# Kernel optimization log

Measured on AMD Instinct MI355X. Metric: run time of the kernel, lower is better.

The kernel has to match this reference:

```python
import jax, jax.numpy as jnp
import numpy as np

N_NODES = 50000
N_EDGES = 800000
IN_FEATS = 256
HEADS = 4
OUT_FEATS = 32
NEG_SLOPE = 0.2


def setup_inputs() -> dict:
    key = jax.random.key(0)
    ks = jax.random.split(key, 8)
    return {
        "feat": jax.random.normal(ks[0], (N_NODES, IN_FEATS), dtype=jnp.float32),
        "edge_weight": jax.random.uniform(ks[1], (N_EDGES,), dtype=jnp.float32),
        "src": jax.random.randint(ks[2], (N_EDGES,), 0, N_NODES, dtype=jnp.int32),
        "dst": jax.random.randint(ks[3], (N_EDGES,), 0, N_NODES, dtype=jnp.int32),
        "W_fc": jax.random.normal(ks[4], (HEADS * OUT_FEATS, IN_FEATS), dtype=jnp.float32) * 0.05,
        "W_edge": jax.random.normal(ks[5], (HEADS * OUT_FEATS, 1), dtype=jnp.float32) * 0.05,
        "attn_l": jax.random.normal(ks[6], (1, HEADS, OUT_FEATS), dtype=jnp.float32) * 0.1,
        "attn_r": jax.random.normal(ks[7], (1, HEADS, OUT_FEATS), dtype=jnp.float32) * 0.1,
        "bias": jnp.zeros((HEADS * OUT_FEATS,), dtype=jnp.float32),
    }


def reference(feat, edge_weight, src, dst, W_fc, W_edge, attn_l, attn_r, bias):
    N = feat.shape[0]
    H, F = attn_l.shape[1], attn_l.shape[2]
    # node projection: [N, H, F]
    feat_hf = (feat @ W_fc.T).reshape(N, H, F)
    el = jnp.sum(feat_hf * attn_l, axis=-1)  # [N, H]
    er = jnp.sum(feat_hf * attn_r, axis=-1)  # [N, H]
    # edgefc(weight.unsqueeze(-1)): Linear(1, H*F) -> weight[e] * W_edge[:,0]
    edge_ft = (edge_weight[:, None] * W_edge[:, 0][None, :]).reshape(-1, H, F)  # [E,H,F]
    # e = leaky_relu(u_add_v(el, er) + edge_ft); broadcast [E,H,1] + [E,H,F]
    e = (el[src] + er[dst])[:, :, None] + edge_ft
    e = jnp.where(e >= 0, e, NEG_SLOPE * e)
    # edge softmax per destination (elementwise over H, F)
    m = jax.ops.segment_max(e, dst, num_segments=N)  # [N,H,F]
    m = jnp.where(jnp.isfinite(m), m, 0.0)
    ex = jnp.exp(e - m[dst])
    s = jax.ops.segment_sum(ex, dst, num_segments=N)  # [N,H,F]
    a = ex / s[dst]
    # weighted aggregation: sum_{e: dst=v} ft[src[e]] * a[e]
    rst = jax.ops.segment_sum(feat_hf[src] * a, dst, num_segments=N)  # [N,H,F]
    rst = rst + bias.reshape(1, H, F)
    return rst
```

## Files before the change

kernel.cpp:

```cpp
#include <hip/hip_runtime.h>

#define NN 50000
#define NE 800000
#define KF 256
#define HF 128
#define NEG 0.2f
#define INVLN2 1.44269504088896340736f

#define NB 391
#define EB 391
#define EPB 2048
#define PREP_BLOCKS 64
#define PROJ_BLOCKS 782
#define ELR_BLOCKS 12500

typedef __attribute__((ext_vector_type(8))) short bf16x8;
typedef __attribute__((ext_vector_type(4))) float f32x4;

static __device__ __forceinline__ unsigned bf16_rne(float x) {
  unsigned u = __float_as_uint(x);
  return (u + 0x7fffu + ((u >> 16) & 1u)) >> 16;
}
static __device__ __forceinline__ unsigned cvt_pk(float lo, float hi) {
  unsigned r;
  asm("v_cvt_pk_bf16_f32 %0, %1, %2" : "=v"(r) : "v"(lo), "v"(hi));
  return r;
}
static __device__ __forceinline__ float exp2_raw(float x) {
  float r;
  asm("v_exp_f32 %0, %1" : "=v"(r) : "v"(x));
  return r;
}

__global__ __launch_bounds__(256) void k1_prep_hist(
    const float* __restrict__ Wfc, unsigned* __restrict__ wfcb,
    const int* __restrict__ dst, unsigned short* __restrict__ rank16,
    int* __restrict__ histE) {
  if (blockIdx.x < PREP_BLOCKS) {
    int t = blockIdx.x * 256 + threadIdx.x;
    int e2 = t & 3;
    int l  = (t >> 2) & 63;
    int ct = (t >> 8) & 7;
    int ks = t >> 11;
    int j = ct * 16 + (l & 15);
    int k = ks * 32 + (l >> 4) * 8 + 2 * e2;
    unsigned lo = bf16_rne(Wfc[j * KF + k]);
    unsigned hi = bf16_rne(Wfc[j * KF + k + 1]);
    wfcb[t] = lo | (hi << 16);
    return;
  }
  int e = blockIdx.x - PREP_BLOCKS;
  __shared__ int hist[NB];
  for (int b = threadIdx.x; b < NB; b += 256) hist[b] = 0;
  __syncthreads();
  int base = e * EPB;
  int cnt = min(EPB, NE - base);
  for (int k = threadIdx.x; k < cnt; k += 256) {
    int d = dst[base + k];
    int r = atomicAdd(&hist[d >> 7], 1);
    rank16[base + k] = (unsigned short)r;
  }
  __syncthreads();
  for (int b = threadIdx.x; b < NB; b += 256) histE[e * NB + b] = hist[b];
}

__global__ __launch_bounds__(256) void k2_proj_scan(
    const float* __restrict__ feat, const unsigned* __restrict__ wfcb,
    unsigned* __restrict__ ftp, const int* __restrict__ histE,
    int* __restrict__ colbase, int* __restrict__ bucketTotal) {
  if (blockIdx.x >= PROJ_BLOCKS) {
    int b = blockIdx.x - PROJ_BLOCKS;
    __shared__ int buf[512];
    int t = threadIdx.x;
    int a0 = (t < EB) ? histE[t * NB + b] : 0;
    int a1 = (t + 256 < EB) ? histE[(t + 256) * NB + b] : 0;
    buf[t] = a0;
    buf[t + 256] = a1;
    __syncthreads();
    for (int o = 1; o < 512; o <<= 1) {
      int x0 = (t >= o) ? buf[t - o] : 0;
      int x1 = buf[t + 256 - o];
      __syncthreads();
      buf[t] += x0;
      buf[t + 256] += x1;
      __syncthreads();
    }
    if (t < EB) colbase[t * NB + b] = buf[t] - a0;
    if (t + 256 < EB) colbase[(t + 256) * NB + b] = buf[t + 256] - a1;
    if (t == 0) bucketTotal[b] = buf[EB - 1];
    return;
  }
  int wid = (blockIdx.x * 256 + threadIdx.x) >> 6;
  if (wid >= NN / 16) return;
  const int lane = threadIdx.x & 63;
  const int m0 = wid * 16;
  const int row = m0 + (lane & 15);
  const int kb = (lane >> 4) * 8;

  f32x4 acc[8];
#pragma unroll
  for (int ct = 0; ct < 8; ct++) acc[ct] = (f32x4){0.f, 0.f, 0.f, 0.f};

  const float4* a4p = (const float4*)(feat + row * KF + kb);
#pragma unroll
  for (int ks = 0; ks < 8; ks++) {
    float4 a0 = a4p[ks * 8];
    float4 a1 = a4p[ks * 8 + 1];
    union { int4 i; bf16x8 s; } ua;
    ua.i = make_int4((int)cvt_pk(a0.x, a0.y), (int)cvt_pk(a0.z, a0.w),
                     (int)cvt_pk(a1.x, a1.y), (int)cvt_pk(a1.z, a1.w));
    bf16x8 af = ua.s;
#pragma unroll
    for (int ct = 0; ct < 8; ct++) {
      union { int4 i; bf16x8 s; } ub;
      ub.i = *(const int4*)&wfcb[((ks * 8 + ct) * 64 + lane) * 4];
      acc[ct] = __builtin_amdgcn_mfma_f32_16x16x32_bf16(af, ub.s, acc[ct], 0, 0, 0);
    }
  }

  const int rbase = m0 + (lane >> 4) * 4;
  const int l15 = lane & 15;
#pragma unroll
  for (int ct2 = 0; ct2 < 4; ct2++) {
#pragma unroll
    for (int r = 0; r < 4; r++) {
      unsigned w = cvt_pk(acc[2 * ct2][r], acc[2 * ct2 + 1][r]);
      ftp[(rbase + r) * 64 + ct2 * 16 + l15] = w;
    }
  }
}

__global__ __launch_bounds__(256) void k3_elr_scan2(
    const unsigned* __restrict__ ftp, const float* __restrict__ al,
    const float* __restrict__ ar, float* __restrict__ el, float* __restrict__ er,
    const int* __restrict__ bucketTotal, int* __restrict__ bucketBase) {
  if (blockIdx.x >= ELR_BLOCKS) {
    __shared__ int buf[512];
    int t = threadIdx.x;
    int a0 = (t < NB) ? bucketTotal[t] : 0;
    int a1 = (t + 256 < NB) ? bucketTotal[t + 256] : 0;
    buf[t] = a0;
    buf[t + 256] = a1;
    __syncthreads();
    for (int o = 1; o < 512; o <<= 1) {
      int x0 = (t >= o) ? buf[t - o] : 0;
      int x1 = buf[t + 256 - o];
      __syncthreads();
      buf[t] += x0;
      buf[t + 256] += x1;
      __syncthreads();
    }
    if (t < NB) bucketBase[t] = buf[t] - a0;
    if (t + 256 < NB) bucketBase[t + 256] = buf[t + 256] - a1;
    if (t == 0) bucketBase[NB] = buf[NB - 1];
    return;
  }
  int v = blockIdx.x * 4 + (threadIdx.x >> 6);
  if (v >= NN) return;
  int lane = threadIdx.x & 63;
  int h = lane >> 4, l15 = lane & 15;
  int c0 = h * 32 + l15, c1 = c0 + 16;
  unsigned u = ftp[v * 64 + lane];
  float f0 = __uint_as_float(u << 16);
  float f1 = __uint_as_float(u & 0xffff0000u);
  float pl = f0 * al[c0] + f1 * al[c1];
  float pr = f0 * ar[c0] + f1 * ar[c1];
#pragma unroll
  for (int o = 1; o < 16; o <<= 1) {
    pl += __shfl_xor(pl, o, 64);
    pr += __shfl_xor(pr, o, 64);
  }
  if (l15 == 0) {
    el[v * 4 + h] = pl * INVLN2;
    er[v * 4 + h] = pr * INVLN2;
  }
}

__global__ __launch_bounds__(256) void k4_scatter(
    const int* __restrict__ dst, const int* __restrict__ src,
    const float* __restrict__ ew, const unsigned short* __restrict__ rank16,
    const int* __restrict__ colbase, const int* __restrict__ bucketBase,
    int2* __restrict__ tmp) {
  __shared__ int sbase[NB];
  int e = blockIdx.x;
  for (int b = threadIdx.x; b < NB; b += 256)
    sbase[b] = bucketBase[b] + colbase[e * NB + b];
  __syncthreads();
  int base = e * EPB;
  int cnt = min(EPB, NE - base);
  for (int k = threadIdx.x; k < cnt; k += 256) {
    int i = base + k;
    int d = dst[i];
    unsigned s = (unsigned)src[i];
    float w = ew[i];
    int pos = sbase[d >> 7] + (int)rank16[i];
    tmp[pos] = make_int2((int)(s | ((unsigned)d << 16)), __float_as_int(w));
  }
}

__global__ __launch_bounds__(256) void k5_bucket(
    const int2* __restrict__ tmp, const int* __restrict__ bucketBase,
    int* __restrict__ segbeg, int* __restrict__ segend, int2* __restrict__ es8) {
  int b = blockIdx.x;
  int ebase = bucketBase[b], eend = bucketBase[b + 1];
  int vbase = b * 128;
  __shared__ int cnt[128], buf[128], cur[128];
  int t = threadIdx.x;
  if (t < 128) cnt[t] = 0;
  __syncthreads();
  for (int i = ebase + t; i < eend; i += 256) {
    unsigned x = (unsigned)tmp[i].x;
    atomicAdd(&cnt[(x >> 16) & 127], 1);
  }
  __syncthreads();
  if (t < 128) buf[t] = cnt[t];
  __syncthreads();
  for (int o = 1; o < 128; o <<= 1) {
    int x = (t < 128 && t >= o) ? buf[t - o] : 0;
    __syncthreads();
    if (t < 128) buf[t] += x;
    __syncthreads();
  }
  if (t < 128) {
    cur[t] = buf[t] - cnt[t];
    int v = vbase + t;
    if (v < NN) {
      segbeg[v] = ebase + cur[t];
      segend[v] = ebase + buf[t];
    }
  }
  __syncthreads();
  for (int i = ebase + t; i < eend; i += 256) {
    int2 rec = tmp[i];
    unsigned x = (unsigned)rec.x;
    int r = atomicAdd(&cur[(x >> 16) & 127], 1);
    es8[ebase + r] = make_int2((int)(x & 0xFFFFu), rec.y);
  }
}

__global__ __launch_bounds__(256) void agg_kernel(
    const unsigned* __restrict__ ftp, const float* __restrict__ el,
    const float* __restrict__ er, const int2* __restrict__ es8,
    const int* __restrict__ segbeg, const int* __restrict__ segend,
    const float* __restrict__ We, const float* __restrict__ bias,
    float* __restrict__ out) {
  int wid = (blockIdx.x * blockDim.x + threadIdx.x) >> 6;
  if (wid >= NN) return;
  const int lane = threadIdx.x & 63;
  const int v = wid;
  int beg = __builtin_amdgcn_readfirstlane(segbeg[v]);
  int end = __builtin_amdgcn_readfirstlane(segend[v]);
  const int h = lane >> 4;
  const int c0 = h * 32 + (lane & 15), c1 = c0 + 16;
  const float wx = We[c0] * INVLN2, wy = We[c1] * INVLN2;
  const float bx = bias[c0], by = bias[c1];
  if (beg == end) {
    out[v * HF + c0] = bx;
    out[v * HF + c1] = by;
    return;
  }
  const float erv = er[v * 4 + h];
  float num0 = 0.f, num1 = 0.f, den0 = 0.f, den1 = 0.f;

#define EDGE(w_, u_, e_)                                            \
  {                                                                 \
    float base = (e_) + erv;                                        \
    float t0 = fmaf((w_), wx, base); t0 = fmaxf(t0, NEG * t0);      \
    float t1 = fmaf((w_), wy, base); t1 = fmaxf(t1, NEG * t1);      \
    float x0 = exp2_raw(t0), x1 = exp2_raw(t1);                     \
    float f0 = __uint_as_float((u_) << 16);                         \
    float f1 = __uint_as_float((u_) & 0xffff0000u);                 \
    num0 = fmaf(f0, x0, num0); den0 += x0;                          \
    num1 = fmaf(f1, x1, num1); den1 += x1;                          \
  }

  int i = beg;
  for (; i + 8 <= end; i += 8) {
    int2 q0 = es8[i],     q1 = es8[i + 1], q2 = es8[i + 2], q3 = es8[i + 3];
    int2 q4 = es8[i + 4], q5 = es8[i + 5], q6 = es8[i + 6], q7 = es8[i + 7];
    int s0 = __builtin_amdgcn_readfirstlane(q0.x);
    int s1 = __builtin_amdgcn_readfirstlane(q1.x);
    int s2 = __builtin_amdgcn_readfirstlane(q2.x);
    int s3 = __builtin_amdgcn_readfirstlane(q3.x);
    int s4 = __builtin_amdgcn_readfirstlane(q4.x);
    int s5 = __builtin_amdgcn_readfirstlane(q5.x);
    int s6 = __builtin_amdgcn_readfirstlane(q6.x);
    int s7 = __builtin_amdgcn_readfirstlane(q7.x);
    unsigned u0 = ftp[s0 * 64 + lane], u1 = ftp[s1 * 64 + lane];
    unsigned u2 = ftp[s2 * 64 + lane], u3 = ftp[s3 * 64 + lane];
    unsigned u4 = ftp[s4 * 64 + lane], u5 = ftp[s5 * 64 + lane];
    unsigned u6 = ftp[s6 * 64 + lane], u7 = ftp[s7 * 64 + lane];
    float e0 = el[s0 * 4 + h], e1 = el[s1 * 4 + h];
    float e2 = el[s2 * 4 + h], e3 = el[s3 * 4 + h];
    float e4 = el[s4 * 4 + h], e5 = el[s5 * 4 + h];
    float e6 = el[s6 * 4 + h], e7 = el[s7 * 4 + h];
    float w0 = __uint_as_float(__builtin_amdgcn_readfirstlane(q0.y));
    float w1 = __uint_as_float(__builtin_amdgcn_readfirstlane(q1.y));
    float w2 = __uint_as_float(__builtin_amdgcn_readfirstlane(q2.y));
    float w3 = __uint_as_float(__builtin_amdgcn_readfirstlane(q3.y));
    float w4 = __uint_as_float(__builtin_amdgcn_readfirstlane(q4.y));
    float w5 = __uint_as_float(__builtin_amdgcn_readfirstlane(q5.y));
    float w6 = __uint_as_float(__builtin_amdgcn_readfirstlane(q6.y));
    float w7 = __uint_as_float(__builtin_amdgcn_readfirstlane(q7.y));
    EDGE(w0, u0, e0); EDGE(w1, u1, e1); EDGE(w2, u2, e2); EDGE(w3, u3, e3);
    EDGE(w4, u4, e4); EDGE(w5, u5, e5); EDGE(w6, u6, e6); EDGE(w7, u7, e7);
  }
  for (; i < end; i++) {
    int2 q = es8[i];
    int s = __builtin_amdgcn_readfirstlane(q.x);
    unsigned u = ftp[s * 64 + lane];
    float ee = el[s * 4 + h];
    float w = __uint_as_float(__builtin_amdgcn_readfirstlane(q.y));
    EDGE(w, u, ee);
  }
#undef EDGE

  out[v * HF + c0] = num0 / den0 + bx;
  out[v * HF + c1] = num1 / den1 + by;
}

extern "C" void kernel_launch(void* const* d_in, const int* in_sizes, int n_in,
                              void* d_out, int out_size, void* d_ws, size_t ws_size,
                              hipStream_t stream) {
  const float* feat = (const float*)d_in[0];
  const float* ew   = (const float*)d_in[1];
  const int*   src  = (const int*)d_in[2];
  const int*   dst  = (const int*)d_in[3];
  const float* Wfc  = (const float*)d_in[4];
  const float* We   = (const float*)d_in[5];
  const float* al   = (const float*)d_in[6];
  const float* ar   = (const float*)d_in[7];
  const float* bias = (const float*)d_in[8];
  float* out = (float*)d_out;

  char* ws = (char*)d_ws;
  unsigned* ftp        = (unsigned*)(ws + 0);
  float* el            = (float*)(ws + 12800000);
  float* er            = (float*)(ws + 13600000);
  int* segbeg          = (int*)(ws + 14400000);
  int* segend          = (int*)(ws + 14600000);
  int2* es8            = (int2*)(ws + 14800000);
  int2* tmp            = (int2*)(ws + 21200000);
  unsigned short* rank = (unsigned short*)(ws + 27600000);
  int* histE           = (int*)(ws + 29200000);
  int* colbase         = (int*)(ws + 29811524);
  int* bucketTotal     = (int*)(ws + 30423048);
  int* bucketBase      = (int*)(ws + 30424612);
  unsigned* wfcb       = (unsigned*)(ws + 30426192);

  k1_prep_hist<<<PREP_BLOCKS + EB, 256, 0, stream>>>(Wfc, wfcb, dst, rank, histE);
  k2_proj_scan<<<PROJ_BLOCKS + NB, 256, 0, stream>>>(feat, wfcb, ftp, histE, colbase,
                                                     bucketTotal);
  k3_elr_scan2<<<ELR_BLOCKS + 1, 256, 0, stream>>>(ftp, al, ar, el, er, bucketTotal,
                                                   bucketBase);
  k4_scatter<<<EB, 256, 0, stream>>>(dst, src, ew, rank, colbase, bucketBase, tmp);
  k5_bucket<<<NB, 256, 0, stream>>>(tmp, bucketBase, segbeg, segend, es8);
  agg_kernel<<<(NN * 64) / 256, 256, 0, stream>>>(ftp, el, er, es8, segbeg, segend, We,
                                                  bias, out);
}
```

Before: 94.49 us.

## Fuse el/er into projection epilogue, fold bucket scan into scatter, pipeline agg loads

Computes the attention logits el/er in the MFMA projection epilogue, right after packing to bf16, using shuffle reductions. This removes the separate k3 kernel and its re-read of ftp. The bucket-total prefix scan is now recomputed redundantly in every k4_scatter block, with block 0 writing bucketBase, which saves one launch at the cost of extra per-block scan work. The aggregation kernel gains a double-buffered software pipeline that prefetches edge records and gathers for the next group of 8 while computing the current one. It also sets a launch-bounds occupancy hint, with some risk of higher register pressure.

```diff
diff --git a/kernel.cpp b/kernel.cpp
--- a/kernel.cpp
+++ b/kernel.cpp
@@ -12,7 +12,6 @@
 #define EPB 2048
 #define PREP_BLOCKS 64
 #define PROJ_BLOCKS 782
-#define ELR_BLOCKS 12500
 
 typedef __attribute__((ext_vector_type(8))) short bf16x8;
 typedef __attribute__((ext_vector_type(4))) float f32x4;
@@ -67,7 +66,9 @@
 __global__ __launch_bounds__(256) void k2_proj_scan(
     const float* __restrict__ feat, const unsigned* __restrict__ wfcb,
     unsigned* __restrict__ ftp, const int* __restrict__ histE,
-    int* __restrict__ colbase, int* __restrict__ bucketTotal) {
+    int* __restrict__ colbase, int* __restrict__ bucketTotal,
+    const float* __restrict__ al, const float* __restrict__ ar,
+    float* __restrict__ el, float* __restrict__ er) {
   if (blockIdx.x >= PROJ_BLOCKS) {
     int b = blockIdx.x - PROJ_BLOCKS;
     __shared__ int buf[512];
@@ -120,71 +121,79 @@
 
   const int rbase = m0 + (lane >> 4) * 4;
   const int l15 = lane & 15;
+  float alv0[4], alv1[4], arv0[4], arv1[4];
+#pragma unroll
+  for (int t2 = 0; t2 < 4; t2++) {
+    alv0[t2] = al[t2 * 32 + l15];
+    alv1[t2] = al[t2 * 32 + 16 + l15];
+    arv0[t2] = ar[t2 * 32 + l15];
+    arv1[t2] = ar[t2 * 32 + 16 + l15];
+  }
+  float pl_[4][4], pr_[4][4];
 #pragma unroll
   for (int ct2 = 0; ct2 < 4; ct2++) {
 #pragma unroll
     for (int r = 0; r < 4; r++) {
-      unsigned w = cvt_pk(acc[2 * ct2][r], acc[2 * ct2 + 1][r]);
-      ftp[(rbase + r) * 64 + ct2 * 16 + l15] = w;
-    }
-  }
-}
-
-__global__ __launch_bounds__(256) void k3_elr_scan2(
-    const unsigned* __restrict__ ftp, const float* __restrict__ al,
-    const float* __restrict__ ar, float* __restrict__ el, float* __restrict__ er,
-    const int* __restrict__ bucketTotal, int* __restrict__ bucketBase) {
-  if (blockIdx.x >= ELR_BLOCKS) {
-    __shared__ int buf[512];
-    int t = threadIdx.x;
-    int a0 = (t < NB) ? bucketTotal[t] : 0;
-    int a1 = (t + 256 < NB) ? bucketTotal[t + 256] : 0;
-    buf[t] = a0;
-    buf[t + 256] = a1;
-    __syncthreads();
-    for (int o = 1; o < 512; o <<= 1) {
-      int x0 = (t >= o) ? buf[t - o] : 0;
-      int x1 = buf[t + 256 - o];
-      __syncthreads();
-      buf[t] += x0;
-      buf[t + 256] += x1;
-      __syncthreads();
-    }
+      unsigned wv = cvt_pk(acc[2 * ct2][r], acc[2 * ct2 + 1][r]);
+      ftp[(rbase + r) * 64 + ct2 * 16 + l15] = wv;
+      float f0 = __uint_as_float(wv << 16);
+      float f1 = __uint_as_float(wv & 0xffff0000u);
+      pl_[r][ct2] = f0 * alv0[ct2] + f1 * alv1[ct2];
+      pr_[r][ct2] = f0 * arv0[ct2] + f1 * arv1[ct2];
+    }
+  }
+#pragma unroll
+  for (int o = 1; o < 16; o <<= 1) {
+#pragma unroll
+    for (int r = 0; r < 4; r++) {
+#pragma unroll
+      for (int hh = 0; hh < 4; hh++) {
+        pl_[r][hh] += __shfl_xor(pl_[r][hh], o, 64);
+        pr_[r][hh] += __shfl_xor(pr_[r][hh], o, 64);
+      }
+    }
+  }
+  if (l15 == 0) {
+#pragma unroll
+    for (int r = 0; r < 4; r++) {
+#pragma unroll
+      for (int hh = 0; hh < 4; hh++) {
+        el[(rbase + r) * 4 + hh] = pl_[r][hh] * INVLN2;
+        er[(rbase + r) * 4 + hh] = pr_[r][hh] * INVLN2;
+      }
+    }
+  }
+}
+
+__global__ __launch_bounds__(256) void k4_scatter(
+    const int* __restrict__ dst, const int* __restrict__ src,
+    const float* __restrict__ ew, const unsigned short* __restrict__ rank16,
+    const int* __restrict__ colbase, const int* __restrict__ bucketTotal,
+    int* __restrict__ bucketBase, int2* __restrict__ tmp) {
+  __shared__ int sbase[NB];
+  __shared__ int buf[512];
+  int t = threadIdx.x;
+  int e = blockIdx.x;
+  int a0 = (t < NB) ? bucketTotal[t] : 0;
+  int a1 = (t + 256 < NB) ? bucketTotal[t + 256] : 0;
+  buf[t] = a0;
+  buf[t + 256] = a1;
+  __syncthreads();
+  for (int o = 1; o < 512; o <<= 1) {
+    int x0 = (t >= o) ? buf[t - o] : 0;
+    int x1 = buf[t + 256 - o];
+    __syncthreads();
+    buf[t] += x0;
+    buf[t + 256] += x1;
+    __syncthreads();
+  }
+  if (t < NB) sbase[t] = (buf[t] - a0) + colbase[e * NB + t];
+  if (t + 256 < NB) sbase[t + 256] = (buf[t + 256] - a1) + colbase[e * NB + t + 256];
+  if (e == 0) {
     if (t < NB) bucketBase[t] = buf[t] - a0;
     if (t + 256 < NB) bucketBase[t + 256] = buf[t + 256] - a1;
     if (t == 0) bucketBase[NB] = buf[NB - 1];
-    return;
-  }
-  int v = blockIdx.x * 4 + (threadIdx.x >> 6);
-  if (v >= NN) return;
-  int lane = threadIdx.x & 63;
-  int h = lane >> 4, l15 = lane & 15;
-  int c0 = h * 32 + l15, c1 = c0 + 16;
-  unsigned u = ftp[v * 64 + lane];
-  float f0 = __uint_as_float(u << 16);
-  float f1 = __uint_as_float(u & 0xffff0000u);
-  float pl = f0 * al[c0] + f1 * al[c1];
-  float pr = f0 * ar[c0] + f1 * ar[c1];
-#pragma unroll
-  for (int o = 1; o < 16; o <<= 1) {
-    pl += __shfl_xor(pl, o, 64);
-    pr += __shfl_xor(pr, o, 64);
-  }
-  if (l15 == 0) {
-    el[v * 4 + h] = pl * INVLN2;
-    er[v * 4 + h] = pr * INVLN2;
-  }
-}
-
-__global__ __launch_bounds__(256) void k4_scatter(
-    const int* __restrict__ dst, const int* __restrict__ src,
-    const float* __restrict__ ew, const unsigned short* __restrict__ rank16,
-    const int* __restrict__ colbase, const int* __restrict__ bucketBase,
-    int2* __restrict__ tmp) {
-  __shared__ int sbase[NB];
-  int e = blockIdx.x;
-  for (int b = threadIdx.x; b < NB; b += 256)
-    sbase[b] = bucketBase[b] + colbase[e * NB + b];
+  }
   __syncthreads();
   int base = e * EPB;
   int cnt = min(EPB, NE - base);
@@ -238,7 +247,7 @@
   }
 }
 
-__global__ __launch_bounds__(256) void agg_kernel(
+__global__ __launch_bounds__(256, 5) void agg_kernel(
     const unsigned* __restrict__ ftp, const float* __restrict__ el,
     const float* __restrict__ er, const int2* __restrict__ es8,
     const int* __restrict__ segbeg, const int* __restrict__ segend,
@@ -274,36 +283,52 @@
     num1 = fmaf(f1, x1, num1); den1 += x1;                          \
   }
 
+  int2 qv[2][8];
+  int sv[2][8];
+  float wv_[2][8];
+  unsigned uf[2][8];
+  float ev[2][8];
+
+#define QL(P, base_)                                                            \
+  {                                                                             \
+    _Pragma("unroll") for (int j = 0; j < 8; j++) qv[P][j] = es8[(base_) + j];  \
+  }
+#define XG(P)                                                                        \
+  {                                                                                  \
+    _Pragma("unroll") for (int j = 0; j < 8; j++) {                                  \
+      sv[P][j] = __builtin_amdgcn_readfirstlane(qv[P][j].x);                         \
+      wv_[P][j] = __uint_as_float(__builtin_amdgcn_readfirstlane(qv[P][j].y));       \
+    }                                                                                \
+    _Pragma("unroll") for (int j = 0; j < 8; j++) {                                  \
+      uf[P][j] = ftp[sv[P][j] * 64 + lane];                                          \
+      ev[P][j] = el[sv[P][j] * 4 + h];                                               \
+    }                                                                                \
+  }
+#define CP(P)                                                                        \
+  {                                                                                  \
+    _Pragma("unroll") for (int j = 0; j < 8; j++)                                    \
+        EDGE(wv_[P][j], uf[P][j], ev[P][j]);                                         \
+  }
+
+  int nf = (end - beg) >> 3;
   int i = beg;
-  for (; i + 8 <= end; i += 8) {
-    int2 q0 = es8[i],     q1 = es8[i + 1], q2 = es8[i + 2], q3 = es8[i + 3];
-    int2 q4 = es8[i + 4], q5 = es8[i + 5], q6 = es8[i + 6], q7 = es8[i + 7];
-    int s0 = __builtin_amdgcn_readfirstlane(q0.x);
-    int s1 = __builtin_amdgcn_readfirstlane(q1.x);
-    int s2 = __builtin_amdgcn_readfirstlane(q2.x);
-    int s3 = __builtin_amdgcn_readfirstlane(q3.x);
-    int s4 = __builtin_amdgcn_readfirstlane(q4.x);
-    int s5 = __builtin_amdgcn_readfirstlane(q5.x);
-    int s6 = __builtin_amdgcn_readfirstlane(q6.x);
-    int s7 = __builtin_amdgcn_readfirstlane(q7.x);
-    unsigned u0 = ftp[s0 * 64 + lane], u1 = ftp[s1 * 64 + lane];
-    unsigned u2 = ftp[s2 * 64 + lane], u3 = ftp[s3 * 64 + lane];
-    unsigned u4 = ftp[s4 * 64 + lane], u5 = ftp[s5 * 64 + lane];
-    unsigned u6 = ftp[s6 * 64 + lane], u7 = ftp[s7 * 64 + lane];
-    float e0 = el[s0 * 4 + h], e1 = el[s1 * 4 + h];
-    float e2 = el[s2 * 4 + h], e3 = el[s3 * 4 + h];
-    float e4 = el[s4 * 4 + h], e5 = el[s5 * 4 + h];
-    float e6 = el[s6 * 4 + h], e7 = el[s7 * 4 + h];
-    float w0 = __uint_as_float(__builtin_amdgcn_readfirstlane(q0.y));
-    float w1 = __uint_as_float(__builtin_amdgcn_readfirstlane(q1.y));
-    float w2 = __uint_as_float(__builtin_amdgcn_readfirstlane(q2.y));
-    float w3 = __uint_as_float(__builtin_amdgcn_readfirstlane(q3.y));
-    float w4 = __uint_as_float(__builtin_amdgcn_readfirstlane(q4.y));
-    float w5 = __uint_as_float(__builtin_amdgcn_readfirstlane(q5.y));
-    float w6 = __uint_as_float(__builtin_amdgcn_readfirstlane(q6.y));
-    float w7 = __uint_as_float(__builtin_amdgcn_readfirstlane(q7.y));
-    EDGE(w0, u0, e0); EDGE(w1, u1, e1); EDGE(w2, u2, e2); EDGE(w3, u3, e3);
-    EDGE(w4, u4, e4); EDGE(w5, u5, e5); EDGE(w6, u6, e6); EDGE(w7, u7, e7);
+  if (nf > 0) {
+    QL(0, i);
+    if (nf > 1) QL(1, i + 8);
+    XG(0);
+    int k = 0;
+    for (;;) {
+      if (k + 2 < nf) QL(0, i + 16);
+      if (k + 1 < nf) XG(1);
+      CP(0);
+      i += 8; k++;
+      if (k == nf) break;
+      if (k + 2 < nf) QL(1, i + 16);
+      if (k + 1 < nf) XG(0);
+      CP(1);
+      i += 8; k++;
+      if (k == nf) break;
+    }
   }
   for (; i < end; i++) {
     int2 q = es8[i];
@@ -314,6 +339,9 @@
     EDGE(w, u, ee);
   }
 #undef EDGE
+#undef QL
+#undef XG
+#undef CP
 
   out[v * HF + c0] = num0 / den0 + bx;
   out[v * HF + c1] = num1 / den1 + by;
@@ -350,10 +378,9 @@
 
   k1_prep_hist<<<PREP_BLOCKS + EB, 256, 0, stream>>>(Wfc, wfcb, dst, rank, histE);
   k2_proj_scan<<<PROJ_BLOCKS + NB, 256, 0, stream>>>(feat, wfcb, ftp, histE, colbase,
-                                                     bucketTotal);
-  k3_elr_scan2<<<ELR_BLOCKS + 1, 256, 0, stream>>>(ftp, al, ar, el, er, bucketTotal,
-                                                   bucketBase);
-  k4_scatter<<<EB, 256, 0, stream>>>(dst, src, ew, rank, colbase, bucketBase, tmp);
+                                                     bucketTotal, al, ar, el, er);
+  k4_scatter<<<EB, 256, 0, stream>>>(dst, src, ew, rank, colbase, bucketTotal,
+                                     bucketBase, tmp);
   k5_bucket<<<NB, 256, 0, stream>>>(tmp, bucketBase, segbeg, segend, es8);
   agg_kernel<<<(NN * 64) / 256, 256, 0, stream>>>(ftp, el, er, es8, segbeg, segend, We,
                                                   bias, out);
```

Result: no change. 95.23 us (+0.8%).

## Replace two-level bucket sort with per-node atomic counting CSR build

Applied to the files above, without the earlier changes.

Edge sorting by destination now uses global per-node atomic counters to assign ranks, instead of per-block bucket histograms followed by a second bucket pass. This removes the tmp buffer and the k5 bucket kernel, so edges are scattered directly into final CSR order. The el/er attention dot products move into the projection kernel epilogue, which removes the separate k3 launch, and the bucket-base scan is recomputed redundantly in each scatter block. The cost is global atomic contention on the node counters, an extra memset, and a nondeterministic edge order within each segment.

```diff
diff --git a/kernel.cpp b/kernel.cpp
--- a/kernel.cpp
+++ b/kernel.cpp
@@ -12,7 +12,6 @@
 #define EPB 2048
 #define PREP_BLOCKS 64
 #define PROJ_BLOCKS 782
-#define ELR_BLOCKS 12500
 
 typedef __attribute__((ext_vector_type(8))) short bf16x8;
 typedef __attribute__((ext_vector_type(4))) float f32x4;
@@ -35,7 +34,7 @@
 __global__ __launch_bounds__(256) void k1_prep_hist(
     const float* __restrict__ Wfc, unsigned* __restrict__ wfcb,
     const int* __restrict__ dst, unsigned short* __restrict__ rank16,
-    int* __restrict__ histE) {
+    int* __restrict__ nodeCnt) {
   if (blockIdx.x < PREP_BLOCKS) {
     int t = blockIdx.x * 256 + threadIdx.x;
     int e2 = t & 3;
@@ -50,44 +49,40 @@
     return;
   }
   int e = blockIdx.x - PREP_BLOCKS;
-  __shared__ int hist[NB];
-  for (int b = threadIdx.x; b < NB; b += 256) hist[b] = 0;
-  __syncthreads();
   int base = e * EPB;
   int cnt = min(EPB, NE - base);
   for (int k = threadIdx.x; k < cnt; k += 256) {
-    int d = dst[base + k];
-    int r = atomicAdd(&hist[d >> 7], 1);
-    rank16[base + k] = (unsigned short)r;
-  }
-  __syncthreads();
-  for (int b = threadIdx.x; b < NB; b += 256) histE[e * NB + b] = hist[b];
+    int i = base + k;
+    int d = dst[i];
+    rank16[i] = (unsigned short)atomicAdd(&nodeCnt[d], 1);
+  }
 }
 
 __global__ __launch_bounds__(256) void k2_proj_scan(
     const float* __restrict__ feat, const unsigned* __restrict__ wfcb,
-    unsigned* __restrict__ ftp, const int* __restrict__ histE,
-    int* __restrict__ colbase, int* __restrict__ bucketTotal) {
+    unsigned* __restrict__ ftp, const int* __restrict__ nodeCnt,
+    int* __restrict__ segLocal, int* __restrict__ bucketTotal,
+    const float* __restrict__ al, const float* __restrict__ ar,
+    float* __restrict__ el, float* __restrict__ er) {
   if (blockIdx.x >= PROJ_BLOCKS) {
     int b = blockIdx.x - PROJ_BLOCKS;
-    __shared__ int buf[512];
+    __shared__ int buf[128];
     int t = threadIdx.x;
-    int a0 = (t < EB) ? histE[t * NB + b] : 0;
-    int a1 = (t + 256 < EB) ? histE[(t + 256) * NB + b] : 0;
-    buf[t] = a0;
-    buf[t + 256] = a1;
+    int v = b * 128 + t;
+    int c = 0;
+    if (t < 128) {
+      c = (v < NN) ? nodeCnt[v] : 0;
+      buf[t] = c;
+    }
     __syncthreads();
-    for (int o = 1; o < 512; o <<= 1) {
-      int x0 = (t >= o) ? buf[t - o] : 0;
-      int x1 = buf[t + 256 - o];
+    for (int o = 1; o < 128; o <<= 1) {
+      int x = (t < 128 && t >= o) ? buf[t - o] : 0;
       __syncthreads();
-      buf[t] += x0;
-      buf[t + 256] += x1;
+      if (t < 128) buf[t] += x;
       __syncthreads();
     }
-    if (t < EB) colbase[t * NB + b] = buf[t] - a0;
-    if (t + 256 < EB) colbase[(t + 256) * NB + b] = buf[t + 256] - a1;
-    if (t == 0) bucketTotal[b] = buf[EB - 1];
+    if (t < 128 && v < NN) segLocal[v] = buf[t] - c;
+    if (t == 0) bucketTotal[b] = buf[127];
     return;
   }
   int wid = (blockIdx.x * 256 + threadIdx.x) >> 6;
@@ -120,121 +115,91 @@
 
   const int rbase = m0 + (lane >> 4) * 4;
   const int l15 = lane & 15;
+  float alv0[4], alv1[4], arv0[4], arv1[4];
+#pragma unroll
+  for (int t2 = 0; t2 < 4; t2++) {
+    alv0[t2] = al[t2 * 32 + l15];
+    alv1[t2] = al[t2 * 32 + 16 + l15];
+    arv0[t2] = ar[t2 * 32 + l15];
+    arv1[t2] = ar[t2 * 32 + 16 + l15];
+  }
+  float pl_[4][4], pr_[4][4];
 #pragma unroll
   for (int ct2 = 0; ct2 < 4; ct2++) {
 #pragma unroll
     for (int r = 0; r < 4; r++) {
-      unsigned w = cvt_pk(acc[2 * ct2][r], acc[2 * ct2 + 1][r]);
-      ftp[(rbase + r) * 64 + ct2 * 16 + l15] = w;
-    }
-  }
-}
-
-__global__ __launch_bounds__(256) void k3_elr_scan2(
-    const unsigned* __restrict__ ftp, const float* __restrict__ al,
-    const float* __restrict__ ar, float* __restrict__ el, float* __restrict__ er,
-    const int* __restrict__ bucketTotal, int* __restrict__ bucketBase) {
-  if (blockIdx.x >= ELR_BLOCKS) {
-    __shared__ int buf[512];
-    int t = threadIdx.x;
-    int a0 = (t < NB) ? bucketTotal[t] : 0;
-    int a1 = (t + 256 < NB) ? bucketTotal[t + 256] : 0;
-    buf[t] = a0;
-    buf[t + 256] = a1;
-    __syncthreads();
-    for (int o = 1; o < 512; o <<= 1) {
-      int x0 = (t >= o) ? buf[t - o] : 0;
-      int x1 = buf[t + 256 - o];
-      __syncthreads();
-      buf[t] += x0;
-      buf[t + 256] += x1;
-      __syncthreads();
-    }
-    if (t < NB) bucketBase[t] = buf[t] - a0;
-    if (t + 256 < NB) bucketBase[t + 256] = buf[t + 256] - a1;
-    if (t == 0) bucketBase[NB] = buf[NB - 1];
-    return;
-  }
-  int v = blockIdx.x * 4 + (threadIdx.x >> 6);
-  if (v >= NN) return;
-  int lane = threadIdx.x & 63;
-  int h = lane >> 4, l15 = lane & 15;
-  int c0 = h * 32 + l15, c1 = c0 + 16;
-  unsigned u = ftp[v * 64 + lane];
-  float f0 = __uint_as_float(u << 16);
-  float f1 = __uint_as_float(u & 0xffff0000u);
-  float pl = f0 * al[c0] + f1 * al[c1];
-  float pr = f0 * ar[c0] + f1 * ar[c1];
+      unsigned wv = cvt_pk(acc[2 * ct2][r], acc[2 * ct2 + 1][r]);
+      ftp[(rbase + r) * 64 + ct2 * 16 + l15] = wv;
+      float f0 = __uint_as_float(wv << 16);
+      float f1 = __uint_as_float(wv & 0xffff0000u);
+      pl_[r][ct2] = f0 * alv0[ct2] + f1 * alv1[ct2];
+      pr_[r][ct2] = f0 * arv0[ct2] + f1 * arv1[ct2];
+    }
+  }
 #pragma unroll
   for (int o = 1; o < 16; o <<= 1) {
-    pl += __shfl_xor(pl, o, 64);
-    pr += __shfl_xor(pr, o, 64);
+#pragma unroll
+    for (int r = 0; r < 4; r++) {
+#pragma unroll
+      for (int hh = 0; hh < 4; hh++) {
+        pl_[r][hh] += __shfl_xor(pl_[r][hh], o, 64);
+        pr_[r][hh] += __shfl_xor(pr_[r][hh], o, 64);
+      }
+    }
   }
   if (l15 == 0) {
-    el[v * 4 + h] = pl * INVLN2;
-    er[v * 4 + h] = pr * INVLN2;
+#pragma unroll
+    for (int r = 0; r < 4; r++) {
+#pragma unroll
+      for (int hh = 0; hh < 4; hh++) {
+        el[(rbase + r) * 4 + hh] = pl_[r][hh] * INVLN2;
+        er[(rbase + r) * 4 + hh] = pr_[r][hh] * INVLN2;
+      }
+    }
   }
 }
 
 __global__ __launch_bounds__(256) void k4_scatter(
     const int* __restrict__ dst, const int* __restrict__ src,
     const float* __restrict__ ew, const unsigned short* __restrict__ rank16,
-    const int* __restrict__ colbase, const int* __restrict__ bucketBase,
-    int2* __restrict__ tmp) {
-  __shared__ int sbase[NB];
+    const int* __restrict__ segLocal, const int* __restrict__ nodeCnt,
+    const int* __restrict__ bucketTotal, int* __restrict__ segbeg,
+    int* __restrict__ segend, int2* __restrict__ es8) {
+  __shared__ int buf[512];
+  __shared__ int bb[NB];
+  int t = threadIdx.x;
   int e = blockIdx.x;
-  for (int b = threadIdx.x; b < NB; b += 256)
-    sbase[b] = bucketBase[b] + colbase[e * NB + b];
+  int a0 = (t < NB) ? bucketTotal[t] : 0;
+  int a1 = (t + 256 < NB) ? bucketTotal[t + 256] : 0;
+  buf[t] = a0;
+  buf[t + 256] = a1;
   __syncthreads();
+  for (int o = 1; o < 512; o <<= 1) {
+    int x0 = (t >= o) ? buf[t - o] : 0;
+    int x1 = buf[t + 256 - o];
+    __syncthreads();
+    buf[t] += x0;
+    buf[t + 256] += x1;
+    __syncthreads();
+  }
+  if (t < NB) bb[t] = buf[t] - a0;
+  if (t + 256 < NB) bb[t + 256] = buf[t + 256] - a1;
+  __syncthreads();
+  if (t < 128) {
+    int v = e * 128 + t;
+    if (v < NN) {
+      int sb = bb[e] + segLocal[v];
+      segbeg[v] = sb;
+      segend[v] = sb + nodeCnt[v];
+    }
+  }
   int base = e * EPB;
   int cnt = min(EPB, NE - base);
-  for (int k = threadIdx.x; k < cnt; k += 256) {
+  for (int k = t; k < cnt; k += 256) {
     int i = base + k;
     int d = dst[i];
-    unsigned s = (unsigned)src[i];
-    float w = ew[i];
-    int pos = sbase[d >> 7] + (int)rank16[i];
-    tmp[pos] = make_int2((int)(s | ((unsigned)d << 16)), __float_as_int(w));
-  }
-}
-
-__global__ __launch_bounds__(256) void k5_bucket(
-    const int2* __restrict__ tmp, const int* __restrict__ bucketBase,
-    int* __restrict__ segbeg, int* __restrict__ segend, int2* __restrict__ es8) {
-  int b = blockIdx.x;
-  int ebase = bucketBase[b], eend = bucketBase[b + 1];
-  int vbase = b * 128;
-  __shared__ int cnt[128], buf[128], cur[128];
-  int t = threadIdx.x;
-  if (t < 128) cnt[t] = 0;
-  __syncthreads();
-  for (int i = ebase + t; i < eend; i += 256) {
-    unsigned x = (unsigned)tmp[i].x;
-    atomicAdd(&cnt[(x >> 16) & 127], 1);
-  }
-  __syncthreads();
-  if (t < 128) buf[t] = cnt[t];
-  __syncthreads();
-  for (int o = 1; o < 128; o <<= 1) {
-    int x = (t < 128 && t >= o) ? buf[t - o] : 0;
-    __syncthreads();
-    if (t < 128) buf[t] += x;
-    __syncthreads();
-  }
-  if (t < 128) {
-    cur[t] = buf[t] - cnt[t];
-    int v = vbase + t;
-    if (v < NN) {
-      segbeg[v] = ebase + cur[t];
-      segend[v] = ebase + buf[t];
-    }
-  }
-  __syncthreads();
-  for (int i = ebase + t; i < eend; i += 256) {
-    int2 rec = tmp[i];
-    unsigned x = (unsigned)rec.x;
-    int r = atomicAdd(&cur[(x >> 16) & 127], 1);
-    es8[ebase + r] = make_int2((int)(x & 0xFFFFu), rec.y);
+    int pos = bb[d >> 7] + segLocal[d] + (int)rank16[i];
+    es8[pos] = make_int2(src[i], __float_as_int(ew[i]));
   }
 }
 
@@ -340,21 +305,18 @@
   int* segbeg          = (int*)(ws + 14400000);
   int* segend          = (int*)(ws + 14600000);
   int2* es8            = (int2*)(ws + 14800000);
-  int2* tmp            = (int2*)(ws + 21200000);
-  unsigned short* rank = (unsigned short*)(ws + 27600000);
-  int* histE           = (int*)(ws + 29200000);
-  int* colbase         = (int*)(ws + 29811524);
-  int* bucketTotal     = (int*)(ws + 30423048);
-  int* bucketBase      = (int*)(ws + 30424612);
-  unsigned* wfcb       = (unsigned*)(ws + 30426192);
-
-  k1_prep_hist<<<PREP_BLOCKS + EB, 256, 0, stream>>>(Wfc, wfcb, dst, rank, histE);
-  k2_proj_scan<<<PROJ_BLOCKS + NB, 256, 0, stream>>>(feat, wfcb, ftp, histE, colbase,
-                                                     bucketTotal);
-  k3_elr_scan2<<<ELR_BLOCKS + 1, 256, 0, stream>>>(ftp, al, ar, el, er, bucketTotal,
-                                                   bucketBase);
-  k4_scatter<<<EB, 256, 0, stream>>>(dst, src, ew, rank, colbase, bucketBase, tmp);
-  k5_bucket<<<NB, 256, 0, stream>>>(tmp, bucketBase, segbeg, segend, es8);
+  int* segLocal        = (int*)(ws + 21200000);
+  int* nodeCnt         = (int*)(ws + 21400000);
+  int* bucketTotal     = (int*)(ws + 21600000);
+  unsigned short* rank = (unsigned short*)(ws + 21601568);
+  unsigned* wfcb       = (unsigned*)(ws + 23201568);
+
+  hipMemsetAsync(nodeCnt, 0, NN * sizeof(int), stream);
+  k1_prep_hist<<<PREP_BLOCKS + EB, 256, 0, stream>>>(Wfc, wfcb, dst, rank, nodeCnt);
+  k2_proj_scan<<<PROJ_BLOCKS + NB, 256, 0, stream>>>(feat, wfcb, ftp, nodeCnt, segLocal,
+                                                     bucketTotal, al, ar, el, er);
+  k4_scatter<<<EB, 256, 0, stream>>>(dst, src, ew, rank, segLocal, nodeCnt, bucketTotal,
+                                     segbeg, segend, es8);
   agg_kernel<<<(NN * 64) / 256, 256, 0, stream>>>(ftp, el, er, es8, segbeg, segend, We,
                                                   bias, out);
 }
```

Result: slower. 122.8 us (+30.0%).

## Fuse el/er into projection, move bucket scan into scatter, drop rank array

Applied to the files above, without the earlier changes.

The attention dot products el/er are now computed in the projection kernel's epilogue straight from the MFMA accumulators, so the separate elr kernel and its re-read of ftp go away. The global bucket prefix scan is recomputed redundantly in every scatter block, and the per-edge rank is regenerated with shared-memory atomics instead of being stored to a 16-bit array. The histogram is also stored transposed so the column scan reads contiguous memory. This removes one kernel launch and some global traffic, at the cost of redundant scans, extra shuffles in the projection, and atomics in the scatter. The rank order within a bucket is now nondeterministic, but the bucket sort should still be correct.

```diff
diff --git a/kernel.cpp b/kernel.cpp
--- a/kernel.cpp
+++ b/kernel.cpp
@@ -12,7 +12,6 @@
 #define EPB 2048
 #define PREP_BLOCKS 64
 #define PROJ_BLOCKS 782
-#define ELR_BLOCKS 12500
 
 typedef __attribute__((ext_vector_type(8))) short bf16x8;
 typedef __attribute__((ext_vector_type(4))) float f32x4;
@@ -34,8 +33,7 @@
 
 __global__ __launch_bounds__(256) void k1_prep_hist(
     const float* __restrict__ Wfc, unsigned* __restrict__ wfcb,
-    const int* __restrict__ dst, unsigned short* __restrict__ rank16,
-    int* __restrict__ histE) {
+    const int* __restrict__ dst, int* __restrict__ histT) {
   if (blockIdx.x < PREP_BLOCKS) {
     int t = blockIdx.x * 256 + threadIdx.x;
     int e2 = t & 3;
@@ -57,23 +55,24 @@
   int cnt = min(EPB, NE - base);
   for (int k = threadIdx.x; k < cnt; k += 256) {
     int d = dst[base + k];
-    int r = atomicAdd(&hist[d >> 7], 1);
-    rank16[base + k] = (unsigned short)r;
-  }
-  __syncthreads();
-  for (int b = threadIdx.x; b < NB; b += 256) histE[e * NB + b] = hist[b];
+    atomicAdd(&hist[d >> 7], 1);
+  }
+  __syncthreads();
+  for (int b = threadIdx.x; b < NB; b += 256) histT[b * EB + e] = hist[b];
 }
 
 __global__ __launch_bounds__(256) void k2_proj_scan(
     const float* __restrict__ feat, const unsigned* __restrict__ wfcb,
-    unsigned* __restrict__ ftp, const int* __restrict__ histE,
-    int* __restrict__ colbase, int* __restrict__ bucketTotal) {
+    unsigned* __restrict__ ftp, const int* __restrict__ histT,
+    int* __restrict__ colbase, int* __restrict__ bucketTotal,
+    const float* __restrict__ al, const float* __restrict__ ar,
+    float* __restrict__ el, float* __restrict__ er) {
   if (blockIdx.x >= PROJ_BLOCKS) {
     int b = blockIdx.x - PROJ_BLOCKS;
     __shared__ int buf[512];
     int t = threadIdx.x;
-    int a0 = (t < EB) ? histE[t * NB + b] : 0;
-    int a1 = (t + 256 < EB) ? histE[(t + 256) * NB + b] : 0;
+    int a0 = (t < EB) ? histT[b * EB + t] : 0;
+    int a1 = (t + 256 < EB) ? histT[b * EB + t + 256] : 0;
     buf[t] = a0;
     buf[t + 256] = a1;
     __syncthreads();
@@ -120,80 +119,95 @@
 
   const int rbase = m0 + (lane >> 4) * 4;
   const int l15 = lane & 15;
+  float alv0[4], alv1[4], arv0[4], arv1[4];
+#pragma unroll
+  for (int t2 = 0; t2 < 4; t2++) {
+    alv0[t2] = al[t2 * 32 + l15];
+    alv1[t2] = al[t2 * 32 + 16 + l15];
+    arv0[t2] = ar[t2 * 32 + l15];
+    arv1[t2] = ar[t2 * 32 + 16 + l15];
+  }
+  float pl_[4][4], pr_[4][4];
 #pragma unroll
   for (int ct2 = 0; ct2 < 4; ct2++) {
 #pragma unroll
     for (int r = 0; r < 4; r++) {
-      unsigned w = cvt_pk(acc[2 * ct2][r], acc[2 * ct2 + 1][r]);
-      ftp[(rbase + r) * 64 + ct2 * 16 + l15] = w;
-    }
-  }
-}
-
-__global__ __launch_bounds__(256) void k3_elr_scan2(
-    const unsigned* __restrict__ ftp, const float* __restrict__ al,
-    const float* __restrict__ ar, float* __restrict__ el, float* __restrict__ er,
-    const int* __restrict__ bucketTotal, int* __restrict__ bucketBase) {
-  if (blockIdx.x >= ELR_BLOCKS) {
-    __shared__ int buf[512];
-    int t = threadIdx.x;
-    int a0 = (t < NB) ? bucketTotal[t] : 0;
-    int a1 = (t + 256 < NB) ? bucketTotal[t + 256] : 0;
-    buf[t] = a0;
-    buf[t + 256] = a1;
-    __syncthreads();
-    for (int o = 1; o < 512; o <<= 1) {
-      int x0 = (t >= o) ? buf[t - o] : 0;
-      int x1 = buf[t + 256 - o];
-      __syncthreads();
-      buf[t] += x0;
-      buf[t + 256] += x1;
-      __syncthreads();
-    }
-    if (t < NB) bucketBase[t] = buf[t] - a0;
-    if (t + 256 < NB) bucketBase[t + 256] = buf[t + 256] - a1;
-    if (t == 0) bucketBase[NB] = buf[NB - 1];
-    return;
-  }
-  int v = blockIdx.x * 4 + (threadIdx.x >> 6);
-  if (v >= NN) return;
-  int lane = threadIdx.x & 63;
-  int h = lane >> 4, l15 = lane & 15;
-  int c0 = h * 32 + l15, c1 = c0 + 16;
-  unsigned u = ftp[v * 64 + lane];
-  float f0 = __uint_as_float(u << 16);
-  float f1 = __uint_as_float(u & 0xffff0000u);
-  float pl = f0 * al[c0] + f1 * al[c1];
-  float pr = f0 * ar[c0] + f1 * ar[c1];
+      unsigned wv = cvt_pk(acc[2 * ct2][r], acc[2 * ct2 + 1][r]);
+      ftp[(rbase + r) * 64 + ct2 * 16 + l15] = wv;
+      float f0 = __uint_as_float(wv << 16);
+      float f1 = __uint_as_float(wv & 0xffff0000u);
+      pl_[r][ct2] = f0 * alv0[ct2] + f1 * alv1[ct2];
+      pr_[r][ct2] = f0 * arv0[ct2] + f1 * arv1[ct2];
+    }
+  }
 #pragma unroll
   for (int o = 1; o < 16; o <<= 1) {
-    pl += __shfl_xor(pl, o, 64);
-    pr += __shfl_xor(pr, o, 64);
+#pragma unroll
+    for (int r = 0; r < 4; r++) {
+#pragma unroll
+      for (int hh = 0; hh < 4; hh++) {
+        pl_[r][hh] += __shfl_xor(pl_[r][hh], o, 64);
+        pr_[r][hh] += __shfl_xor(pr_[r][hh], o, 64);
+      }
+    }
   }
   if (l15 == 0) {
-    el[v * 4 + h] = pl * INVLN2;
-    er[v * 4 + h] = pr * INVLN2;
+#pragma unroll
+    for (int r = 0; r < 4; r++) {
+#pragma unroll
+      for (int hh = 0; hh < 4; hh++) {
+        el[(rbase + r) * 4 + hh] = pl_[r][hh] * INVLN2;
+        er[(rbase + r) * 4 + hh] = pr_[r][hh] * INVLN2;
+      }
+    }
   }
 }
 
 __global__ __launch_bounds__(256) void k4_scatter(
     const int* __restrict__ dst, const int* __restrict__ src,
-    const float* __restrict__ ew, const unsigned short* __restrict__ rank16,
-    const int* __restrict__ colbase, const int* __restrict__ bucketBase,
+    const float* __restrict__ ew, const int* __restrict__ colbase,
+    const int* __restrict__ bucketTotal, int* __restrict__ bucketBase,
     int2* __restrict__ tmp) {
+  __shared__ int buf[512];
   __shared__ int sbase[NB];
+  __shared__ int lcnt[NB];
+  int t = threadIdx.x;
   int e = blockIdx.x;
-  for (int b = threadIdx.x; b < NB; b += 256)
-    sbase[b] = bucketBase[b] + colbase[e * NB + b];
+  int a0 = (t < NB) ? bucketTotal[t] : 0;
+  int a1 = (t + 256 < NB) ? bucketTotal[t + 256] : 0;
+  buf[t] = a0;
+  buf[t + 256] = a1;
+  for (int b = t; b < NB; b += 256) lcnt[b] = 0;
+  __syncthreads();
+  for (int o = 1; o < 512; o <<= 1) {
+    int x0 = (t >= o) ? buf[t - o] : 0;
+    int x1 = buf[t + 256 - o];
+    __syncthreads();
+    buf[t] += x0;
+    buf[t + 256] += x1;
+    __syncthreads();
+  }
+  if (t < NB) {
+    int bb0 = buf[t] - a0;
+    sbase[t] = bb0 + colbase[e * NB + t];
+    if (e == 0) bucketBase[t] = bb0;
+  }
+  if (t + 256 < NB) {
+    int bb1 = buf[t + 256] - a1;
+    sbase[t + 256] = bb1 + colbase[e * NB + t + 256];
+    if (e == 0) bucketBase[t + 256] = bb1;
+  }
+  if (e == 0 && t == 0) bucketBase[NB] = buf[NB - 1];
   __syncthreads();
   int base = e * EPB;
   int cnt = min(EPB, NE - base);
-  for (int k = threadIdx.x; k < cnt; k += 256) {
+  for (int k = t; k < cnt; k += 256) {
     int i = base + k;
     int d = dst[i];
     unsigned s = (unsigned)src[i];
     float w = ew[i];
-    int pos = sbase[d >> 7] + (int)rank16[i];
+    int r = atomicAdd(&lcnt[d >> 7], 1);
+    int pos = sbase[d >> 7] + r;
     tmp[pos] = make_int2((int)(s | ((unsigned)d << 16)), __float_as_int(w));
   }
 }
@@ -341,19 +355,17 @@
   int* segend          = (int*)(ws + 14600000);
   int2* es8            = (int2*)(ws + 14800000);
   int2* tmp            = (int2*)(ws + 21200000);
-  unsigned short* rank = (unsigned short*)(ws + 27600000);
-  int* histE           = (int*)(ws + 29200000);
-  int* colbase         = (int*)(ws + 29811524);
-  int* bucketTotal     = (int*)(ws + 30423048);
-  int* bucketBase      = (int*)(ws + 30424612);
-  unsigned* wfcb       = (unsigned*)(ws + 30426192);
-
-  k1_prep_hist<<<PREP_BLOCKS + EB, 256, 0, stream>>>(Wfc, wfcb, dst, rank, histE);
-  k2_proj_scan<<<PROJ_BLOCKS + NB, 256, 0, stream>>>(feat, wfcb, ftp, histE, colbase,
-                                                     bucketTotal);
-  k3_elr_scan2<<<ELR_BLOCKS + 1, 256, 0, stream>>>(ftp, al, ar, el, er, bucketTotal,
-                                                   bucketBase);
-  k4_scatter<<<EB, 256, 0, stream>>>(dst, src, ew, rank, colbase, bucketBase, tmp);
+  int* histT           = (int*)(ws + 27600000);
+  int* colbase         = (int*)(ws + 28211524);
+  int* bucketTotal     = (int*)(ws + 28823048);
+  int* bucketBase      = (int*)(ws + 28824612);
+  unsigned* wfcb       = (unsigned*)(ws + 28826180);
+
+  k1_prep_hist<<<PREP_BLOCKS + EB, 256, 0, stream>>>(Wfc, wfcb, dst, histT);
+  k2_proj_scan<<<PROJ_BLOCKS + NB, 256, 0, stream>>>(feat, wfcb, ftp, histT, colbase,
+                                                     bucketTotal, al, ar, el, er);
+  k4_scatter<<<EB, 256, 0, stream>>>(dst, src, ew, colbase, bucketTotal, bucketBase,
+                                     tmp);
   k5_bucket<<<NB, 256, 0, stream>>>(tmp, bucketBase, segbeg, segend, es8);
   agg_kernel<<<(NN * 64) / 256, 256, 0, stream>>>(ftp, el, er, es8, segbeg, segend, We,
                                                   bias, out);
```

Result: faster. 91.40 us (-3.3%).
